# Performance work log

Measured on AMD Instinct MI355X. Metric: run time of the kernel, lower is better.

Reference implementation:

```python
import jax, jax.numpy as jnp
import numpy as np

N, F, H, C = 50000, 128, 256, 40
E = 800000
L, J = 3, 2
TOT = 7  # sum_{i<L} J**i


def setup_inputs() -> dict:
    key = jax.random.key(0)
    ks = jax.random.split(key, 16)
    def rn(k, shape, scale):
        return jax.random.normal(k, shape, jnp.float32) * scale
    w = lambda k, shape: rn(k, shape, 1.0 / np.sqrt(shape[0]).astype(np.float32))
    return {
        "x": rn(ks[0], (N, F), 1.0),
        "feature": rn(ks[1], (TOT, N, F), 1.0),
        "src": jax.random.randint(ks[2], (E,), 0, N),
        "dst": jax.random.randint(ks[3], (E,), 0, N),
        "conv_W0": w(ks[4], (F, H)),       "conv_b0": jnp.zeros((H,), jnp.float32),
        "conv_W1": w(ks[5], (2 * H, H)),   "conv_b1": jnp.zeros((H,), jnp.float32),
        "conv_W2": w(ks[6], (2 * H, H)),   "conv_b2": jnp.zeros((H,), jnp.float32),
        "lin_W0": w(ks[7], (F, H)),        "lin_b0": jnp.zeros((H,), jnp.float32),
        "lin_W1": w(ks[8], (2 * F, H)),    "lin_b1": jnp.zeros((H,), jnp.float32),
        "lin_W2": w(ks[9], (4 * F, H)),    "lin_b2": jnp.zeros((H,), jnp.float32),
        "order_weights": rn(ks[10], (J,), 1.0 / np.sqrt(J).astype(np.float32)),
        "cls_W": w(ks[11], (2 * H, C)),    "cls_b": jnp.zeros((C,), jnp.float32),
    }


def reference(x, feature, src, dst,
              conv_W0, conv_b0, conv_W1, conv_b1, conv_W2, conv_b2,
              lin_W0, lin_b0, lin_W1, lin_b1, lin_W2, lin_b2,
              order_weights, cls_W, cls_b):
    # GCN normalization with self-loops (A-hat = D^-1/2 (A+I) D^-1/2)
    loop = jnp.arange(N, dtype=src.dtype)
    src_sl = jnp.concatenate([src, loop])   # [E+N]
    dst_sl = jnp.concatenate([dst, loop])
    deg = jax.ops.segment_sum(jnp.ones_like(dst_sl, jnp.float32), dst_sl, num_segments=N)
    dinv = jax.lax.rsqrt(deg)  # deg >= 1 thanks to self loops
    norm = dinv[src_sl] * dinv[dst_sl]      # [E+N]

    def gcn(h, W, b):
        m = h @ W                            # transform first (smaller gather)
        agg = jax.ops.segment_sum(m[src_sl] * norm[:, None], dst_sl, num_segments=N)
        return agg + b

    conv_W = [conv_W0, conv_W1, conv_W2]
    conv_b = [conv_b0, conv_b1, conv_b2]
    lin_W = [lin_W0, lin_W1, lin_W2]
    lin_b = [lin_b0, lin_b1, lin_b2]

    comb = x
    begin = 0
    for i in range(L):
        convx = jax.nn.relu(gcn(comb, conv_W[i], conv_b[i]))  # [N, H]
        count = J ** i
        lf = feature[begin:begin + count]                      # [count, N, F]
        if i > 0:
            ow = jnp.tile(order_weights, J ** (i - 1)).reshape(-1, 1, 1)
            lf = ow * lf
        lf = jnp.moveaxis(lf, 0, 1).reshape(N, count * F)      # [N, count*F]
        lin_sct = jax.nn.relu(lf @ lin_W[i] + lin_b[i])        # [N, H]
        comb = jnp.concatenate([lin_sct, convx], axis=-1)      # [N, 2H]
        begin += count
    logits = gcn(comb, cls_W, cls_b)                           # [N, C]
    return jax.nn.log_softmax(logits, axis=-1), logits
```

## Files before the change

kernel.cpp:

```cpp
#include <hip/hip_runtime.h>

#define DEVI __device__ __forceinline__

namespace {

constexpr int Nn = 50000;
constexpr int Ne = 800000;
constexpr int Fd = 128;
constexpr int Hd = 256;
constexpr int Cd = 40;
constexpr int NB = (Nn + 255) / 256;

typedef __attribute__((ext_vector_type(8))) short s16x8;
typedef __attribute__((ext_vector_type(8))) unsigned short u16x8;
typedef __attribute__((ext_vector_type(4))) float f32x4;
typedef __attribute__((ext_vector_type(4))) unsigned int u32x4;

DEVI unsigned short f2bf(float f) {
  unsigned int u = __builtin_bit_cast(unsigned int, f);
  u += 0x7fffu + ((u >> 16) & 1u);
  return (unsigned short)(u >> 16);
}
DEVI float bf2f(unsigned short s) {
  return __builtin_bit_cast(float, ((unsigned int)s) << 16);
}
DEVI unsigned cvtpk(float lo, float hi) {
  unsigned r;
  asm("v_cvt_pk_bf16_f32 %0, %1, %2" : "=v"(r) : "v"(lo), "v"(hi));
  return r;
}

DEVI void gld_lds16(const void* gptr, void* lds_base) {
  const unsigned m0v =
      (unsigned)__builtin_amdgcn_readfirstlane((unsigned)(uintptr_t)lds_base);
  asm volatile("s_mov_b32 m0, %0\n\t"
               "global_load_lds_dwordx4 %1, off"
               :: "s"(m0v), "v"(gptr) : "memory");
}

DEVI void wt_one(const float* __restrict__ W, unsigned short* __restrict__ Wt,
                 int idx, int K, int H, const float* __restrict__ ow) {
  int c = idx / K, k = idx - c * K;
  int kt = k >> 6, c16 = (k >> 3) & 7, j = k & 7;
  int ksrc = (kt << 6) | ((c16 ^ (c & 7)) << 3) | j;
  float v = (c < H) ? W[(size_t)ksrc * H + c] : 0.0f;
  if (ow) v *= ow[(ksrc >> 7) & 1];
  Wt[idx] = f2bf(v);
}

constexpr int WTO0 = 0;
constexpr int WTO1 = WTO0 + 256 * 128;
constexpr int WTO2 = WTO1 + 256 * 512;
constexpr int WTO3 = WTO2 + 256 * 512;
constexpr int WTO4 = WTO3 + 256 * 128;
constexpr int WTO5 = WTO4 + 256 * 256;
constexpr int WTO6 = WTO5 + 256 * 512;
constexpr int WTO7 = WTO6 + 64 * 512;
constexpr int PREPTOT = WTO7 + Nn;

__global__ __launch_bounds__(256) void k_prep(
    const float* W0, const float* W1, const float* W2, const float* W3,
    const float* W4, const float* W5, const float* W6, const float* ow,
    unsigned short* T0, unsigned short* T1, unsigned short* T2, unsigned short* T3,
    unsigned short* T4, unsigned short* T5, unsigned short* T6, int* cnt) {
  int idx = blockIdx.x * 256 + threadIdx.x;
  if (idx >= PREPTOT) return;
  if (idx < WTO1)      wt_one(W0, T0, idx - WTO0, 128, 256, nullptr);
  else if (idx < WTO2) wt_one(W1, T1, idx - WTO1, 512, 256, nullptr);
  else if (idx < WTO3) wt_one(W2, T2, idx - WTO2, 512, 256, nullptr);
  else if (idx < WTO4) wt_one(W3, T3, idx - WTO3, 128, 256, nullptr);
  else if (idx < WTO5) wt_one(W4, T4, idx - WTO4, 256, 256, ow);
  else if (idx < WTO6) wt_one(W5, T5, idx - WTO5, 512, 256, ow);
  else if (idx < WTO7) wt_one(W6, T6, idx - WTO6, 512, 40, nullptr);
  else cnt[idx - WTO7] = 0;
}

__global__ void k_count(const int* __restrict__ dst, int* __restrict__ cnt) {
  int e = blockIdx.x * 256 + threadIdx.x;
  if (e < Ne) atomicAdd(&cnt[dst[e]], 1);
}

__global__ __launch_bounds__(256) void k_partial(const int* __restrict__ cnt,
                                                 int* __restrict__ partial) {
  __shared__ int red[256];
  const int t = threadIdx.x;
  const int i = blockIdx.x * 256 + t;
  red[t] = (i < Nn) ? cnt[i] + 1 : 0;
  __syncthreads();
#pragma unroll
  for (int off = 128; off; off >>= 1) {
    if (t < off) red[t] += red[t + off];
    __syncthreads();
  }
  if (t == 0) partial[blockIdx.x] = red[0];
}

__global__ __launch_bounds__(256) void k_scan_small(const int* __restrict__ partial,
                                                    int* __restrict__ poffs,
                                                    int* __restrict__ rowptr) {
  __shared__ int s[256];
  const int t = threadIdx.x;
  const int v = (t < NB) ? partial[t] : 0;
  s[t] = v;
  __syncthreads();
#pragma unroll
  for (int off = 1; off < 256; off <<= 1) {
    int add = (t >= off) ? s[t - off] : 0;
    __syncthreads();
    s[t] += add;
    __syncthreads();
  }
  if (t < NB) poffs[t] = s[t] - v;
  if (t == NB - 1) rowptr[Nn] = s[t];
}

__global__ __launch_bounds__(256) void k_rowptr(const int* __restrict__ cnt,
                                                const int* __restrict__ poffs,
                                                int* __restrict__ rowptr,
                                                int* __restrict__ cursor,
                                                float* __restrict__ dinv) {
  __shared__ int s[256];
  const int t = threadIdx.x;
  const int i = blockIdx.x * 256 + t;
  const int c = (i < Nn) ? cnt[i] + 1 : 0;
  s[t] = c;
  __syncthreads();
#pragma unroll
  for (int off = 1; off < 256; off <<= 1) {
    int add = (t >= off) ? s[t - off] : 0;
    __syncthreads();
    s[t] += add;
    __syncthreads();
  }
  if (i < Nn) {
    const int excl = s[t] - c + poffs[blockIdx.x];
    rowptr[i] = excl;
    cursor[i] = excl;
    dinv[i] = rsqrtf((float)c);
  }
}

__global__ void k_fill(const int* __restrict__ src, const int* __restrict__ dst,
                       const float* __restrict__ dinv, int* __restrict__ cursor,
                       int* __restrict__ csrs, float* __restrict__ csrn) {
  int e = blockIdx.x * 256 + threadIdx.x;
  if (e < Ne) {
    int s = src[e], d = dst[e];
    int pos = atomicAdd(&cursor[d], 1);
    csrs[pos] = s;
    csrn[pos] = dinv[s] * dinv[d];
  } else if (e < Ne + Nn) {
    int d = e - Ne;
    int pos = atomicAdd(&cursor[d], 1);
    csrs[pos] = d;
    float v = dinv[d];
    csrn[pos] = v * v;
  }
}

struct GRole {
  const float* A;
  const unsigned short* Wt;
  const float* bias;
  unsigned short* C;
  int K;
  int ldc;
  int relu;
};

__global__ __launch_bounds__(256) void k_gemm4(GRole R0, GRole R1, GRole R2, GRole R3) {
  const GRole R = (blockIdx.y == 0) ? R0 : (blockIdx.y == 1) ? R1
                  : (blockIdx.y == 2) ? R2 : R3;
  __shared__ char smem[49152];
  short* lA0 = (short*)smem;
  short* lA1 = (short*)(smem + 8192);
  short* lB  = (short*)(smem + 16384);
  const int tid = threadIdx.x;
  const int lane = tid & 63;
  const int wid = tid >> 6;
  const int wc = wid;
  const int row0 = blockIdx.x * 64;
  const size_t NnF = (size_t)Nn * Fd;

  f32x4 acc[4][4];
#pragma unroll
  for (int i = 0; i < 4; ++i)
#pragma unroll
    for (int j = 0; j < 4; ++j) acc[i][j] = (f32x4)0.0f;

  auto issueA = [&](int kt, f32x4 (&A4)[2][2]) {
    const int k0 = kt * 64;
    const int c = k0 >> 7;
    const int f0 = k0 & 127;
#pragma unroll
    for (int i = 0; i < 2; ++i) {
      const int v = tid * 2 + i;
      const int row = v >> 3, c16 = v & 7;
      const int grow = row0 + row;
      const bool rv = grow < Nn;
      const float* p = R.A + (size_t)c * NnF + (size_t)grow * Fd + f0 + c16 * 8;
      A4[i][0] = rv ? *(const f32x4*)p : (f32x4)0.0f;
      A4[i][1] = rv ? *(const f32x4*)(p + 4) : (f32x4)0.0f;
    }
  };
  auto writeA = [&](f32x4 (&A4)[2][2], short* lAb) {
#pragma unroll
    for (int i = 0; i < 2; ++i) {
      const int v = tid * 2 + i;
      const int row = v >> 3, c16 = v & 7;
      u32x4 val;
      val.x = cvtpk(A4[i][0][0], A4[i][0][1]);
      val.y = cvtpk(A4[i][0][2], A4[i][0][3]);
      val.z = cvtpk(A4[i][1][0], A4[i][1][1]);
      val.w = cvtpk(A4[i][1][2], A4[i][1][3]);
      int byte = row * 128 + c16 * 16;
      byte ^= (row & 7) << 4;
      *(u32x4*)((char*)lAb + byte) = val;
    }
  };
  auto stageB = [&](int kt) {
    const int k0 = kt * 64;
#pragma unroll
    for (int i = 0; i < 8; ++i) {
      const int iss = wid * 8 + i;
      const int col = iss * 8 + (lane >> 3);
      gld_lds16(R.Wt + (size_t)col * R.K + k0 + (lane & 7) * 8, lB + iss * 512);
    }
  };
  auto readB = [&](s16x8 (&bv)[2][4]) {
#pragma unroll
    for (int kk = 0; kk < 2; ++kk)
#pragma unroll
      for (int ni = 0; ni < 4; ++ni) {
        int c = wc * 64 + ni * 16 + (lane & 15);
        int byte = c * 128 + kk * 64 + (lane >> 4) * 16;
        byte ^= (c & 7) << 4;
        bv[kk][ni] = *(const s16x8*)((const char*)lB + byte);
      }
  };
  auto mfma = [&](const short* lAb, s16x8 (&bv)[2][4]) {
#pragma unroll
    for (int kk = 0; kk < 2; ++kk) {
      s16x8 af[4];
#pragma unroll
      for (int mi = 0; mi < 4; ++mi) {
        int r = mi * 16 + (lane & 15);
        int byte = r * 128 + kk * 64 + (lane >> 4) * 16;
        byte ^= (r & 7) << 4;
        af[mi] = *(const s16x8*)((const char*)lAb + byte);
      }
#pragma unroll
      for (int mi = 0; mi < 4; ++mi)
#pragma unroll
        for (int ni = 0; ni < 4; ++ni)
          acc[mi][ni] = __builtin_amdgcn_mfma_f32_16x16x32_bf16(af[mi], bv[kk][ni], acc[mi][ni], 0, 0, 0);
    }
  };

  const int nkt = R.K >> 6;
  f32x4 Ar0[2][2], Ar1[2][2];
  issueA(0, Ar0);
  stageB(0);
  issueA(1, Ar1);
  writeA(Ar0, lA0);
  asm volatile("s_waitcnt lgkmcnt(0)" ::: "memory");
  __builtin_amdgcn_s_barrier();
  for (int kt = 0; kt < nkt; ++kt) {
    if (kt + 1 < nkt) asm volatile("s_waitcnt vmcnt(4)" ::: "memory");
    else              asm volatile("s_waitcnt vmcnt(0)" ::: "memory");
    s16x8 bv[2][4];
    readB(bv);
    asm volatile("s_waitcnt lgkmcnt(0)" ::: "memory");
    if (kt + 1 < nkt) stageB(kt + 1);
    if (kt + 2 < nkt) {
      if (kt & 1) issueA(kt + 2, Ar1); else issueA(kt + 2, Ar0);
    }
    if (kt + 1 < nkt) {
      if ((kt + 1) & 1) writeA(Ar1, lA1); else writeA(Ar0, lA0);
    }
    mfma((kt & 1) ? lA1 : lA0, bv);
    asm volatile("s_waitcnt lgkmcnt(0)" ::: "memory");
    __builtin_amdgcn_s_barrier();
  }

  short* lC = (short*)smem;
#pragma unroll
  for (int ni = 0; ni < 4; ++ni) {
    const int col = wc * 64 + ni * 16 + (lane & 15);
    const float bvl = R.bias ? R.bias[col] : 0.0f;
#pragma unroll
    for (int mi = 0; mi < 4; ++mi) {
      const int rb = mi * 16 + ((lane >> 4) << 2);
#pragma unroll
      for (int q = 0; q < 4; ++q) {
        float vv = acc[mi][ni][q] + bvl;
        if (R.relu) vv = fmaxf(vv, 0.0f);
        lC[(rb + q) * 264 + col] = f2bf(vv);
      }
    }
  }
  __syncthreads();
#pragma unroll
  for (int p = 0; p < 8; ++p) {
    const int flat = p * 256 + tid;
    const int row = flat >> 5;
    const int ch = flat & 31;
    const int r = row0 + row;
    if (r < Nn)
      *(u16x8*)(R.C + (size_t)r * R.ldc + ch * 8) =
          *(const u16x8*)(lC + row * 264 + ch * 8);
  }
}

__global__ __launch_bounds__(256) void k_gemmC(
    const unsigned short* __restrict__ A, int lda, int K,
    const unsigned short* __restrict__ Wt, unsigned short* __restrict__ C,
    int ldc) {
  __shared__ char smem[81920];
  short* lA0 = (short*)smem;
  short* lA1 = (short*)(smem + 8192);
  short* lB0 = (short*)(smem + 16384);
  short* lB1 = (short*)(smem + 49152);
  const int tid = threadIdx.x;
  const int lane = tid & 63;
  const int wid = tid >> 6;
  const int wc = wid;
  const int row0 = blockIdx.x * 64;
  const int c16a = (lane & 7) ^ ((lane >> 3) & 7);

  f32x4 acc[4][4];
#pragma unroll
  for (int i = 0; i < 4; ++i)
#pragma unroll
    for (int j = 0; j < 4; ++j) acc[i][j] = (f32x4)0.0f;

  auto stage = [&](int kt) {
    short* a = (kt & 1) ? lA1 : lA0;
    short* b = (kt & 1) ? lB1 : lB0;
    const int k0 = kt * 64;
#pragma unroll
    for (int i = 0; i < 2; ++i) {
      const int iss = wid * 2 + i;
      const int row = row0 + iss * 8 + (lane >> 3);
      gld_lds16(A + (size_t)row * lda + k0 + c16a * 8, a + iss * 512);
    }
#pragma unroll
    for (int i = 0; i < 8; ++i) {
      const int iss = wid * 8 + i;
      const int col = iss * 8 + (lane >> 3);
      gld_lds16(Wt + (size_t)col * K + k0 + (lane & 7) * 8, b + iss * 512);
    }
  };
  auto mfma = [&](const short* lAb, const short* lBb) {
#pragma unroll
    for (int kk = 0; kk < 2; ++kk) {
      s16x8 af[4], bv[4];
#pragma unroll
      for (int mi = 0; mi < 4; ++mi) {
        int r = mi * 16 + (lane & 15);
        int byte = r * 128 + kk * 64 + (lane >> 4) * 16;
        byte ^= (r & 7) << 4;
        af[mi] = *(const s16x8*)((const char*)lAb + byte);
      }
#pragma unroll
      for (int ni = 0; ni < 4; ++ni) {
        int c = wc * 64 + ni * 16 + (lane & 15);
        int byte = c * 128 + kk * 64 + (lane >> 4) * 16;
        byte ^= (c & 7) << 4;
        bv[ni] = *(const s16x8*)((const char*)lBb + byte);
      }
#pragma unroll
      for (int mi = 0; mi < 4; ++mi)
#pragma unroll
        for (int ni = 0; ni < 4; ++ni)
          acc[mi][ni] = __builtin_amdgcn_mfma_f32_16x16x32_bf16(af[mi], bv[ni], acc[mi][ni], 0, 0, 0);
    }
  };

  const int nkt = K >> 6;
  stage(0);
  stage(1);
  for (int kt = 0; kt < nkt; ++kt) {
    short* curA = (kt & 1) ? lA1 : lA0;
    short* curB = (kt & 1) ? lB1 : lB0;
    if (kt + 1 < nkt) asm volatile("s_waitcnt vmcnt(10)" ::: "memory");
    else              asm volatile("s_waitcnt vmcnt(0)" ::: "memory");
    __builtin_amdgcn_s_barrier();
    mfma(curA, curB);
    __builtin_amdgcn_s_barrier();
    if (kt + 2 < nkt) stage(kt + 2);
  }

  short* lC = (short*)smem;
#pragma unroll
  for (int ni = 0; ni < 4; ++ni) {
    const int col = wc * 64 + ni * 16 + (lane & 15);
#pragma unroll
    for (int mi = 0; mi < 4; ++mi) {
      const int rb = mi * 16 + ((lane >> 4) << 2);
#pragma unroll
      for (int q = 0; q < 4; ++q)
        lC[(rb + q) * 264 + col] = f2bf(acc[mi][ni][q]);
    }
  }
  __syncthreads();
#pragma unroll
  for (int p = 0; p < 8; ++p) {
    const int flat = p * 256 + tid;
    const int row = flat >> 5;
    const int ch = flat & 31;
    const int r = row0 + row;
    if (r < Nn)
      *(u16x8*)(C + (size_t)r * ldc + ch * 8) =
          *(const u16x8*)(lC + row * 264 + ch * 8);
  }
}

__global__ __launch_bounds__(256) void k_gemmX(
    const unsigned short* __restrict__ A, int lda, int K,
    const unsigned short* __restrict__ Wt, unsigned short* __restrict__ C,
    int ldc, int ncols) {
  __shared__ char smem[81920];
  short* lA0 = (short*)smem;
  short* lA1 = (short*)(smem + 32768);
  short* lB0 = (short*)(smem + 65536);
  short* lB1 = (short*)(smem + 73728);
  const int tid = threadIdx.x;
  const int lane = tid & 63;
  const int wid = tid >> 6;
  const int wr = wid;
  const int row0 = blockIdx.x * 256;
  const int c16a = (lane & 7) ^ ((lane >> 3) & 7);

  f32x4 acc[4][4];
#pragma unroll
  for (int i = 0; i < 4; ++i)
#pragma unroll
    for (int j = 0; j < 4; ++j) acc[i][j] = (f32x4)0.0f;

  auto stage = [&](int kt) {
    short* a = (kt & 1) ? lA1 : lA0;
    short* b = (kt & 1) ? lB1 : lB0;
    const int k0 = kt * 64;
#pragma unroll
    for (int i = 0; i < 8; ++i) {
      const int iss = wid * 8 + i;
      const int row = row0 + iss * 8 + (lane >> 3);
      gld_lds16(A + (size_t)row * lda + k0 + c16a * 8, a + iss * 512);
    }
#pragma unroll
    for (int i = 0; i < 2; ++i) {
      const int iss = wid * 2 + i;
      const int col = iss * 8 + (lane >> 3);
      gld_lds16(Wt + (size_t)col * K + k0 + (lane & 7) * 8, b + iss * 512);
    }
  };
  auto mfma = [&](const short* a, const short* b) {
#pragma unroll
    for (int kk = 0; kk < 2; ++kk) {
      s16x8 af[4], bv[4];
#pragma unroll
      for (int mi = 0; mi < 4; ++mi) {
        int r = wr * 64 + mi * 16 + (lane & 15);
        int byte = r * 128 + kk * 64 + (lane >> 4) * 16;
        byte ^= (r & 7) << 4;
        af[mi] = *(const s16x8*)((const char*)a + byte);
      }
#pragma unroll
      for (int ni = 0; ni < 4; ++ni) {
        int c = ni * 16 + (lane & 15);
        int byte = c * 128 + kk * 64 + (lane >> 4) * 16;
        byte ^= (c & 7) << 4;
        bv[ni] = *(const s16x8*)((const char*)b + byte);
      }
#pragma unroll
      for (int mi = 0; mi < 4; ++mi)
#pragma unroll
        for (int ni = 0; ni < 4; ++ni)
          acc[mi][ni] = __builtin_amdgcn_mfma_f32_16x16x32_bf16(af[mi], bv[ni], acc[mi][ni], 0, 0, 0);
    }
  };

  const int nkt = K >> 6;
  stage(0);
  stage(1);
  for (int kt = 0; kt < nkt; ++kt) {
    short* curA = (kt & 1) ? lA1 : lA0;
    short* curB = (kt & 1) ? lB1 : lB0;
    if (kt + 1 < nkt) asm volatile("s_waitcnt vmcnt(10)" ::: "memory");
    else              asm volatile("s_waitcnt vmcnt(0)" ::: "memory");
    __builtin_amdgcn_s_barrier();
    mfma(curA, curB);
    __builtin_amdgcn_s_barrier();
    if (kt + 2 < nkt) stage(kt + 2);
  }

  short* lC = (short*)smem;
#pragma unroll
  for (int ni = 0; ni < 4; ++ni) {
    const int col = ni * 16 + (lane & 15);
#pragma unroll
    for (int mi = 0; mi < 4; ++mi) {
      const int rb = wr * 64 + mi * 16 + ((lane >> 4) << 2);
#pragma unroll
      for (int q = 0; q < 4; ++q)
        lC[(rb + q) * 72 + col] = f2bf(acc[mi][ni][q]);
    }
  }
  __syncthreads();
#pragma unroll
  for (int p = 0; p < 8; ++p) {
    const int flat = p * 256 + tid;
    const int row = flat >> 3;
    const int ch = flat & 7;
    const int r = row0 + row;
    const int col = ch * 8;
    if (r < Nn && col < ncols)
      *(u16x8*)(C + (size_t)r * ldc + col) = *(const u16x8*)(lC + row * 72 + col);
  }
}

__global__ __launch_bounds__(256) void k_gather(
    const unsigned short* __restrict__ m, const int* __restrict__ rowptr,
    const int* __restrict__ csrs, const float* __restrict__ csrn,
    const float* __restrict__ bias, unsigned short* __restrict__ outp,
    int ldc, int col_off) {
  const int wid = (blockIdx.x * 256 + threadIdx.x) >> 6;
  const int lane = threadIdx.x & 63;
  if (wid >= Nn) return;
  const int half = lane >> 5;
  const int sub = lane & 31;
  const int e0 = rowptr[wid], e1 = rowptr[wid + 1];
  const unsigned short* mcol = m + sub * 8;
  float acc[8];
#pragma unroll
  for (int q = 0; q < 8; ++q) acc[q] = 0.f;

  for (int base = e0; base < e1; base += 64) {
    const int idx = base + lane;
    int s_ = 0;
    float w_ = 0.f;
    if (idx < e1) { s_ = csrs[idx]; w_ = csrn[idx]; }
    const int cn = min(64, e1 - base);
    const int npair = (cn + 1) >> 1;
    float w0, w1, w2, w3;
    u16x8 v0, v1, v2, v3;
    auto pick = [&](int p, float& w, u16x8& v) {
      if (p < npair) {
        const int j = 2 * p + half;
        const int ss = __shfl(s_, j);
        w = __shfl(w_, j);
        v = *(const u16x8*)(mcol + (size_t)ss * Hd);
      } else { w = 0.f; v = (u16x8)0; }
    };
    pick(0, w0, v0); pick(1, w1, v1); pick(2, w2, v2); pick(3, w3, v3);
    for (int p0 = 0; p0 < npair; p0 += 4) {
#pragma unroll
      for (int q = 0; q < 8; ++q) acc[q] += w0 * bf2f(v0[q]);
      pick(p0 + 4, w0, v0);
#pragma unroll
      for (int q = 0; q < 8; ++q) acc[q] += w1 * bf2f(v1[q]);
      pick(p0 + 5, w1, v1);
#pragma unroll
      for (int q = 0; q < 8; ++q) acc[q] += w2 * bf2f(v2[q]);
      pick(p0 + 6, w2, v2);
#pragma unroll
      for (int q = 0; q < 8; ++q) acc[q] += w3 * bf2f(v3[q]);
      pick(p0 + 7, w3, v3);
    }
  }

#pragma unroll
  for (int q = 0; q < 8; ++q) acc[q] += __shfl_xor(acc[q], 32);
  if (half == 0) {
    u16x8 o;
#pragma unroll
    for (int q = 0; q < 8; ++q) {
      float v = fmaxf(acc[q] + bias[sub * 8 + q], 0.f);
      o[q] = f2bf(v);
    }
    *(u16x8*)(outp + (size_t)wid * ldc + col_off + sub * 8) = o;
  }
}

__global__ __launch_bounds__(256) void k_gcls(
    const unsigned short* __restrict__ mc, const int* __restrict__ rowptr,
    const int* __restrict__ csrs, const float* __restrict__ csrn,
    const float* __restrict__ clsb, float* __restrict__ outp) {
  const int wid = (blockIdx.x * 256 + threadIdx.x) >> 6;
  const int lane = threadIdx.x & 63;
  if (wid >= Nn) return;
  const int half = lane >> 5;
  const int sub = lane & 31;
  const bool act = sub < 5;
  const int e0 = rowptr[wid], e1 = rowptr[wid + 1];
  float acc[8];
#pragma unroll
  for (int q = 0; q < 8; ++q) acc[q] = 0.f;

  for (int base = e0; base < e1; base += 64) {
    const int idx = base + lane;
    int s_ = 0;
    float w_ = 0.f;
    if (idx < e1) { s_ = csrs[idx]; w_ = csrn[idx]; }
    const int cn = min(64, e1 - base);
    const int npair = (cn + 1) >> 1;
    int sA = __shfl(s_, half);
    float wA = __shfl(w_, half);
    u16x8 vA = act ? *(const u16x8*)(mc + (size_t)sA * Cd + sub * 8) : (u16x8)0;
    for (int jj = 1; jj < npair; ++jj) {
      const int j = 2 * jj + half;
      const int sB = __shfl(s_, j);
      const float wB = __shfl(w_, j);
      const u16x8 vB = act ? *(const u16x8*)(mc + (size_t)sB * Cd + sub * 8) : (u16x8)0;
#pragma unroll
      for (int q = 0; q < 8; ++q) acc[q] += wA * bf2f(vA[q]);
      wA = wB; vA = vB;
    }
#pragma unroll
    for (int q = 0; q < 8; ++q) acc[q] += wA * bf2f(vA[q]);
  }

#pragma unroll
  for (int q = 0; q < 8; ++q) acc[q] += __shfl_xor(acc[q], 32);

  float l[8];
  float mx = -3.4e38f;
  if (act) {
#pragma unroll
    for (int q = 0; q < 8; ++q) {
      l[q] = acc[q] + clsb[sub * 8 + q];
      mx = fmaxf(mx, l[q]);
    }
  }
#pragma unroll
  for (int off = 1; off < 8; off <<= 1) mx = fmaxf(mx, __shfl_xor(mx, off));
  float se = 0.f;
  if (act) {
#pragma unroll
    for (int q = 0; q < 8; ++q) se += expf(l[q] - mx);
  }
#pragma unroll
  for (int off = 1; off < 8; off <<= 1) se += __shfl_xor(se, off);
  const float lse = mx + logf(se);
  if (half == 0 && act) {
    float* o1 = outp + (size_t)wid * Cd + sub * 8;
    float* o2 = o1 + (size_t)Nn * Cd;
#pragma unroll
    for (int q = 0; q < 8; ++q) {
      o1[q] = l[q] - lse;
      o2[q] = l[q];
    }
  }
}

}

extern "C" void kernel_launch(void* const* d_in, const int* in_sizes, int n_in,
                              void* d_out, int out_size, void* d_ws, size_t ws_size,
                              hipStream_t stream) {
  (void)in_sizes; (void)n_in; (void)out_size; (void)ws_size;
  const float* x       = (const float*)d_in[0];
  const float* feature = (const float*)d_in[1];
  const int* src       = (const int*)d_in[2];
  const int* dst       = (const int*)d_in[3];
  const float* convW[3] = {(const float*)d_in[4], (const float*)d_in[6], (const float*)d_in[8]};
  const float* convB[3] = {(const float*)d_in[5], (const float*)d_in[7], (const float*)d_in[9]};
  const float* linW[3]  = {(const float*)d_in[10], (const float*)d_in[12], (const float*)d_in[14]};
  const float* linB[3]  = {(const float*)d_in[11], (const float*)d_in[13], (const float*)d_in[15]};
  const float* oweights = (const float*)d_in[16];
  const float* clsW     = (const float*)d_in[17];
  const float* clsB     = (const float*)d_in[18];
  float* out = (float*)d_out;

  char* wsp = (char*)d_ws;
  auto alloc = [&](size_t bytes) -> void* {
    void* p = wsp;
    wsp += (bytes + 255) & ~(size_t)255;
    return p;
  };
  int* cnt      = (int*)alloc((size_t)Nn * 4);
  int* cursor   = (int*)alloc((size_t)Nn * 4);
  int* rowptr   = (int*)alloc((size_t)(Nn + 1) * 4);
  float* dinv   = (float*)alloc((size_t)Nn * 4);
  int* partial  = (int*)alloc((size_t)NB * 4);
  int* poffs    = (int*)alloc((size_t)NB * 4);
  int* csrs     = (int*)alloc((size_t)(Ne + Nn) * 4);
  float* csrn   = (float*)alloc((size_t)(Ne + Nn) * 4);
  unsigned short* WtC0 = (unsigned short*)alloc((size_t)256 * 128 * 2);
  unsigned short* WtC1 = (unsigned short*)alloc((size_t)256 * 512 * 2);
  unsigned short* WtC2 = (unsigned short*)alloc((size_t)256 * 512 * 2);
  unsigned short* WtL0 = (unsigned short*)alloc((size_t)256 * 128 * 2);
  unsigned short* WtL1 = (unsigned short*)alloc((size_t)256 * 256 * 2);
  unsigned short* WtL2 = (unsigned short*)alloc((size_t)256 * 512 * 2);
  unsigned short* WtCl = (unsigned short*)alloc((size_t)64 * 512 * 2);
  unsigned short* mbuf = (unsigned short*)alloc((size_t)Nn * Hd * 2);
  unsigned short* mcls = (unsigned short*)alloc((size_t)Nn * Cd * 2);
  unsigned short* comb0 = (unsigned short*)alloc((size_t)(Nn + 256) * 512 * 2);
  unsigned short* comb1 = (unsigned short*)alloc((size_t)(Nn + 256) * 512 * 2);
  unsigned short* comb2 = (unsigned short*)alloc((size_t)(Nn + 256) * 512 * 2);

  k_prep<<<(PREPTOT + 255) / 256, 256, 0, stream>>>(
      convW[0], convW[1], convW[2], linW[0], linW[1], linW[2], clsW, oweights,
      WtC0, WtC1, WtC2, WtL0, WtL1, WtL2, WtCl, cnt);
  k_count<<<(Ne + 255) / 256, 256, 0, stream>>>(dst, cnt);
  k_partial<<<NB, 256, 0, stream>>>(cnt, partial);
  k_scan_small<<<1, 256, 0, stream>>>(partial, poffs, rowptr);
  k_rowptr<<<NB, 256, 0, stream>>>(cnt, poffs, rowptr, cursor, dinv);
  k_fill<<<(Ne + Nn + 255) / 256, 256, 0, stream>>>(src, dst, dinv, cursor, csrs, csrn);

  const int GM = (Nn + 63) / 64;
  const int GC = (Nn + 255) / 256;
  const int GB = (Nn * 64) / 256;

  GRole rConv0{x,                              WtC0, nullptr, mbuf,  128, Hd,  0};
  GRole rLin0 {feature,                        WtL0, linB[0], comb0, 128, 512, 1};
  GRole rLin1 {feature + (size_t)1 * Nn * Fd,  WtL1, linB[1], comb1, 256, 512, 1};
  GRole rLin2 {feature + (size_t)3 * Nn * Fd,  WtL2, linB[2], comb2, 512, 512, 1};
  k_gemm4<<<dim3(GM, 4), 256, 0, stream>>>(rConv0, rLin0, rLin1, rLin2);

  k_gather<<<GB, 256, 0, stream>>>(mbuf, rowptr, csrs, csrn, convB[0], comb0, 512, 256);
  k_gemmC<<<GM, 256, 0, stream>>>(comb0, 512, 512, WtC1, mbuf, Hd);
  k_gather<<<GB, 256, 0, stream>>>(mbuf, rowptr, csrs, csrn, convB[1], comb1, 512, 256);
  k_gemmC<<<GM, 256, 0, stream>>>(comb1, 512, 512, WtC2, mbuf, Hd);
  k_gather<<<GB, 256, 0, stream>>>(mbuf, rowptr, csrs, csrn, convB[2], comb2, 512, 256);
  k_gemmX<<<GC, 256, 0, stream>>>(comb2, 512, 512, WtCl, mcls, Cd, 40);
  k_gcls<<<GB, 256, 0, stream>>>(mcls, rowptr, csrs, csrn, clsB, out);
}
```

Baseline: 486.2 us.

## Deepen A-prefetch to three register stages and interleave gemm4 roles per block

The multi-role GEMM kernel now prefetches A tiles three k-steps ahead using three register buffer sets rather than two, with vmcnt waits adjusted to match. The goal is to hide global-load latency better. The launch grid is also flattened so the four roles (conv0, lin0, lin1, lin2) are interleaved block by block instead of being laid out by blockIdx.y, which spreads the uneven K lengths across CUs. The extra register buffers raise VGPR pressure and may lower occupancy.

Measured after the change: 533.9 us. 1.1x slower.

```diff
diff --git a/kernel.cpp b/kernel.cpp
--- a/kernel.cpp
+++ b/kernel.cpp
@@ -169,8 +169,8 @@
 };
 
 __global__ __launch_bounds__(256) void k_gemm4(GRole R0, GRole R1, GRole R2, GRole R3) {
-  const GRole R = (blockIdx.y == 0) ? R0 : (blockIdx.y == 1) ? R1
-                  : (blockIdx.y == 2) ? R2 : R3;
+  const int role = blockIdx.x & 3;
+  const GRole R = (role == 0) ? R0 : (role == 1) ? R1 : (role == 2) ? R2 : R3;
   __shared__ char smem[49152];
   short* lA0 = (short*)smem;
   short* lA1 = (short*)(smem + 8192);
@@ -179,7 +179,7 @@
   const int lane = tid & 63;
   const int wid = tid >> 6;
   const int wc = wid;
-  const int row0 = blockIdx.x * 64;
+  const int row0 = (blockIdx.x >> 2) * 64;
   const size_t NnF = (size_t)Nn * Fd;
 
   f32x4 acc[4][4];
@@ -258,25 +258,35 @@
   };
 
   const int nkt = R.K >> 6;
-  f32x4 Ar0[2][2], Ar1[2][2];
-  issueA(0, Ar0);
+  f32x4 ArA[2][2], ArB[2][2], ArC[2][2];
+  issueA(0, ArA);
   stageB(0);
-  issueA(1, Ar1);
-  writeA(Ar0, lA0);
+  issueA(1, ArB);
+  if (nkt > 2) issueA(2, ArC);
+  writeA(ArA, lA0);
   asm volatile("s_waitcnt lgkmcnt(0)" ::: "memory");
   __builtin_amdgcn_s_barrier();
   for (int kt = 0; kt < nkt; ++kt) {
-    if (kt + 1 < nkt) asm volatile("s_waitcnt vmcnt(4)" ::: "memory");
-    else              asm volatile("s_waitcnt vmcnt(0)" ::: "memory");
+    const int nwait = ((kt + 1 < nkt) ? 4 : 0) + ((kt + 2 < nkt) ? 4 : 0);
+    if (nwait == 8)      asm volatile("s_waitcnt vmcnt(8)" ::: "memory");
+    else if (nwait == 4) asm volatile("s_waitcnt vmcnt(4)" ::: "memory");
+    else                 asm volatile("s_waitcnt vmcnt(0)" ::: "memory");
     s16x8 bv[2][4];
     readB(bv);
     asm volatile("s_waitcnt lgkmcnt(0)" ::: "memory");
     if (kt + 1 < nkt) stageB(kt + 1);
-    if (kt + 2 < nkt) {
-      if (kt & 1) issueA(kt + 2, Ar1); else issueA(kt + 2, Ar0);
+    if (kt + 3 < nkt) {
+      const int s3 = (kt + 3) % 3;
+      if (s3 == 0) issueA(kt + 3, ArA);
+      else if (s3 == 1) issueA(kt + 3, ArB);
+      else issueA(kt + 3, ArC);
     }
     if (kt + 1 < nkt) {
-      if ((kt + 1) & 1) writeA(Ar1, lA1); else writeA(Ar0, lA0);
+      const int s1 = (kt + 1) % 3;
+      short* nxtA = ((kt + 1) & 1) ? lA1 : lA0;
+      if (s1 == 0) writeA(ArA, nxtA);
+      else if (s1 == 1) writeA(ArB, nxtA);
+      else writeA(ArC, nxtA);
     }
     mfma((kt & 1) ? lA1 : lA0, bv);
     asm volatile("s_waitcnt lgkmcnt(0)" ::: "memory");
@@ -717,7 +727,7 @@
   GRole rLin0 {feature,                        WtL0, linB[0], comb0, 128, 512, 1};
   GRole rLin1 {feature + (size_t)1 * Nn * Fd,  WtL1, linB[1], comb1, 256, 512, 1};
   GRole rLin2 {feature + (size_t)3 * Nn * Fd,  WtL2, linB[2], comb2, 512, 512, 1};
-  k_gemm4<<<dim3(GM, 4), 256, 0, stream>>>(rConv0, rLin0, rLin1, rLin2);
+  k_gemm4<<<GM * 4, 256, 0, stream>>>(rConv0, rLin0, rLin1, rLin2);
 
   k_gather<<<GB, 256, 0, stream>>>(mbuf, rowptr, csrs, csrn, convB[0], comb0, 512, 256);
   k_gemmC<<<GM, 256, 0, stream>>>(comb0, 512, 512, WtC1, mbuf, Hd);
```
